# Kernel tuning notes

Measured on AMD Instinct MI355X. Metric: run time of the kernel, lower is better.

The kernel has to match this reference:

```python
import jax, jax.numpy as jnp
import numpy as np

TOP_K = 2
NUM_EXPERTS = 64
SEQ, BS, HS = 2048, 4, 4096
TOKENS = SEQ * BS  # tokens_per_batch
TOL = 1e-4
EPS = 1e-8


def sinkhorn(temp_cost):
    # temp_cost: (T, E) float32 logits. Mirrors SinkhornRouter.sinkhorn exactly.
    cost = jnp.exp(temp_cost)
    n0, n1 = cost.shape
    # initial d0 (overwritten inside loop in torch too, kept for fidelity of carry dtype/shape)
    d0 = (TOKENS / NUM_EXPERTS) * jnp.sum(jnp.exp(2.0 * temp_cost), axis=1)
    d1 = jnp.ones((n1,), dtype=cost.dtype)
    err0 = jnp.asarray(1e9, dtype=cost.dtype)

    def cond(carry):
        _, _, err = carry
        return err > TOL

    def body(carry):
        d0, d1, _ = carry  # d1 here plays the role of d1_old
        d0_new = (1.0 / n0) / (jnp.sum(d1 * cost, axis=1) + EPS)          # (T,)
        d1_new = (1.0 / n1) / (jnp.sum(d0_new[:, None] * cost, axis=0) + EPS)  # (E,)
        err = jnp.mean(jnp.abs(d1 - d1_new))
        return (d0_new, d1_new, err)

    d0, d1, _ = jax.lax.while_loop(cond, body, (d0, d1, err0))
    return d1 * cost * d0[:, None]


def setup_inputs() -> dict:
    key = jax.random.key(0)
    kx, kw = jax.random.split(key)
    x = jax.random.normal(kx, (SEQ, BS, HS), dtype=jnp.float32)
    W = jax.random.normal(kw, (NUM_EXPERTS, HS), dtype=jnp.float32) * 0.02
    return {"x": x, "W": W}


def reference(x, W):
    # router logits: (T, E)
    logits = jnp.reshape(x, (-1, x.shape[-1])) @ W.T
    # Sinkhorn normalization is done in fp32 under no_grad in torch -> stop_gradient
    norm_logits = sinkhorn(jax.lax.stop_gradient(logits).astype(jnp.float32))
    _, indices = jax.lax.top_k(norm_logits, TOP_K)  # (T, top_k) int32
    # top_k > 1 -> softmax activation (fp32, cast back)
    probs = jax.nn.softmax(logits.astype(jnp.float32), axis=-1).astype(logits.dtype)
    scores = jnp.take_along_axis(probs, indices, axis=1)  # (T, top_k)
    return scores, indices
```

## Files before the change

kernel.cpp:

```cpp
#include <hip/hip_runtime.h>
#include <hip/hip_cooperative_groups.h>
#include <math.h>

namespace cg = cooperative_groups;

namespace {
constexpr int kTokens = 8192;
constexpr int kHS = 4096;
constexpr float kTol = 1e-4f;
constexpr float kEps = 1e-8f;
constexpr int kMaxIters = 1000;
constexpr int kSinkBlocks = 64;
constexpr size_t kTagFloats = 128;
constexpr size_t kGdataFloats = 2 * 64 * 64;
constexpr size_t kPartOff = kTagFloats + kGdataFloats;
constexpr size_t kSliceFloats = (size_t)kTokens * 64;
constexpr size_t kWtpFloats = (size_t)(kHS / 4) * 64 * 4;
}

__device__ __forceinline__ float wave_sum(float v) {
#pragma unroll
  for (int o = 32; o; o >>= 1) v += __shfl_xor(v, o, 64);
  return v;
}

__global__ void __launch_bounds__(128, 2)
k_logits(const float* __restrict__ X, const float* __restrict__ W,
         float* __restrict__ part, int KS) {
  __shared__ float xs[32][132];
  __shared__ float wsh[32][68];
  const int tid = threadIdx.x;
  const int tx = tid & 7;
  const int ty = tid >> 3;
  const int tb = blockIdx.x & 63;
  const int s = blockIdx.x >> 6;
  const int t0 = tb * 128;
  const int k0 = s * KS;
  const int cx = tid & 7;
  const int rx = tid >> 3;

  const float* xsrc = X + (size_t)(t0 + rx) * kHS + k0 + 4 * cx;
  const float* wsrc = W + (size_t)rx * kHS + k0 + 4 * cx;

  float acc[8][8];
#pragma unroll
  for (int i = 0; i < 8; ++i)
#pragma unroll
    for (int j = 0; j < 8; ++j) acc[i][j] = 0.0f;

  const int nkt = KS / 32;
  float4 xa[8], wa[4];
#pragma unroll
  for (int p = 0; p < 8; ++p)
    xa[p] = *(const float4*)(xsrc + (size_t)p * 16 * kHS);
#pragma unroll
  for (int p = 0; p < 4; ++p)
    wa[p] = *(const float4*)(wsrc + (size_t)p * 16 * kHS);

  for (int kt = 0; kt < nkt; ++kt) {
    __syncthreads();
#pragma unroll
    for (int p = 0; p < 8; ++p) {
      xs[4 * cx + 0][rx + 16 * p] = xa[p].x;
      xs[4 * cx + 1][rx + 16 * p] = xa[p].y;
      xs[4 * cx + 2][rx + 16 * p] = xa[p].z;
      xs[4 * cx + 3][rx + 16 * p] = xa[p].w;
    }
#pragma unroll
    for (int p = 0; p < 4; ++p) {
      wsh[4 * cx + 0][rx + 16 * p] = wa[p].x;
      wsh[4 * cx + 1][rx + 16 * p] = wa[p].y;
      wsh[4 * cx + 2][rx + 16 * p] = wa[p].z;
      wsh[4 * cx + 3][rx + 16 * p] = wa[p].w;
    }
    __syncthreads();
    if (kt + 1 < nkt) {
      const int ko = (kt + 1) * 32;
#pragma unroll
      for (int p = 0; p < 8; ++p)
        xa[p] = *(const float4*)(xsrc + (size_t)p * 16 * kHS + ko);
#pragma unroll
      for (int p = 0; p < 4; ++p)
        wa[p] = *(const float4*)(wsrc + (size_t)p * 16 * kHS + ko);
    }
#pragma unroll 8
    for (int k = 0; k < 32; ++k) {
      const float4 x0 = *(const float4*)&xs[k][8 * ty];
      const float4 x1 = *(const float4*)&xs[k][8 * ty + 4];
      const float4 w0 = *(const float4*)&wsh[k][8 * tx];
      const float4 w1 = *(const float4*)&wsh[k][8 * tx + 4];
      const float xr[8] = {x0.x, x0.y, x0.z, x0.w, x1.x, x1.y, x1.z, x1.w};
      const float wr[8] = {w0.x, w0.y, w0.z, w0.w, w1.x, w1.y, w1.z, w1.w};
#pragma unroll
      for (int i = 0; i < 8; ++i)
#pragma unroll
        for (int j = 0; j < 8; ++j) acc[i][j] = fmaf(xr[i], wr[j], acc[i][j]);
    }
  }

  float* pb = part + ((size_t)s * kTokens + t0 + 8 * ty) * 64 + 8 * tx;
#pragma unroll
  for (int i = 0; i < 8; ++i) {
    *(float4*)(pb + (size_t)i * 64) =
        make_float4(acc[i][0], acc[i][1], acc[i][2], acc[i][3]);
    *(float4*)(pb + (size_t)i * 64 + 4) =
        make_float4(acc[i][4], acc[i][5], acc[i][6], acc[i][7]);
  }
}

__global__ void __launch_bounds__(1024, 1)
k_sinkhorn(const float* __restrict__ part, int S, float* __restrict__ out,
           unsigned* __restrict__ tags, float* __restrict__ gdata) {
  const int tid = threadIdx.x;
  const int lane = tid & 63;
  const int wid = __builtin_amdgcn_readfirstlane(tid >> 6);
  const int blk = blockIdx.x;
  __shared__ float lds[1024];

  const int t0 = blk * 128 + wid * 8;
  float lg[8], cst[8];
#pragma unroll
  for (int t = 0; t < 8; ++t) {
    float a = 0.0f;
    for (int s = 0; s < S; ++s)
      a += part[((size_t)s * kTokens + t0 + t) * 64 + lane];
    lg[t] = a;
    cst[t] = expf(a);
  }

  float d1 = 1.0f;
  float d0v[8];
  int buf = 0;
  for (int it = 0; it < kMaxIters; ++it) {
    float p = 0.0f;
#pragma unroll
    for (int t = 0; t < 8; ++t) {
      const float s = wave_sum(d1 * cst[t]);
      const float d0t = (1.0f / 8192.0f) / (s + kEps);
      d0v[t] = d0t;
      p = fmaf(d0t, cst[t], p);
    }
    __syncthreads();
    lds[wid * 64 + lane] = p;
    __syncthreads();
    const unsigned want = (unsigned)(it + 1);
    if (wid == 0) {
      float bp = 0.0f;
#pragma unroll
      for (int w = 0; w < 16; ++w) bp += lds[w * 64 + lane];
      __hip_atomic_store(&gdata[((size_t)buf * 64 + blk) * 64 + lane], bp,
                         __ATOMIC_RELAXED, __HIP_MEMORY_SCOPE_AGENT);
      __threadfence();
      if (lane == 0)
        __hip_atomic_store(&tags[buf * 64 + blk], want, __ATOMIC_RELEASE,
                           __HIP_MEMORY_SCOPE_AGENT);
      while (__hip_atomic_load(&tags[buf * 64 + lane], __ATOMIC_ACQUIRE,
                               __HIP_MEMORY_SCOPE_AGENT) != want) {
        __builtin_amdgcn_s_sleep(1);
      }
    }
    __syncthreads();
    float s2 = 0.0f;
#pragma unroll
    for (int i = 0; i < 4; ++i)
      s2 += __hip_atomic_load(
          &gdata[((size_t)buf * 64 + wid * 4 + i) * 64 + lane],
          __ATOMIC_RELAXED, __HIP_MEMORY_SCOPE_AGENT);
    lds[wid * 64 + lane] = s2;
    __syncthreads();
    float colsum = 0.0f;
#pragma unroll
    for (int w = 0; w < 16; ++w) colsum += lds[w * 64 + lane];
    const float d1n = (1.0f / 64.0f) / (colsum + kEps);
    const float err = wave_sum(fabsf(d1 - d1n)) * (1.0f / 64.0f);
    d1 = d1n;
    buf ^= 1;
    if (err <= kTol) break;
  }

#pragma unroll
  for (int t = 0; t < 8; ++t) {
    const float lgv = lg[t];
    float m = lgv;
#pragma unroll
    for (int o = 32; o; o >>= 1) m = fmaxf(m, __shfl_xor(m, o, 64));
    const float ex = expf(lgv - m);
    const float den = wave_sum(ex);
    const float prob = ex / den;

    const float v = (d1 * cst[t]) * d0v[t];
    float v1 = v;
    int i1 = lane;
#pragma unroll
    for (int o = 32; o; o >>= 1) {
      const float ov = __shfl_xor(v1, o, 64);
      const int oi = __shfl_xor(i1, o, 64);
      if (ov > v1 || (ov == v1 && oi < i1)) { v1 = ov; i1 = oi; }
    }
    float v2 = (lane == i1) ? -INFINITY : v;
    int i2 = lane;
#pragma unroll
    for (int o = 32; o; o >>= 1) {
      const float ov = __shfl_xor(v2, o, 64);
      const int oi = __shfl_xor(i2, o, 64);
      if (ov > v2 || (ov == v2 && oi < i2)) { v2 = ov; i2 = oi; }
    }
    const float p1 = __shfl(prob, i1, 64);
    const float p2 = __shfl(prob, i2, 64);
    if (lane == 0) {
      const int row = t0 + t;
      out[row * 2 + 0] = p1;
      out[row * 2 + 1] = p2;
      out[2 * kTokens + row * 2 + 0] = (float)i1;
      out[2 * kTokens + row * 2 + 1] = (float)i2;
    }
  }
}

__global__ void __launch_bounds__(256, 1)
sinkhorn_router(const float* __restrict__ X, const float* __restrict__ W,
                float* __restrict__ out, float* __restrict__ ws) {
  cg::grid_group grid = cg::this_grid();
  const int tid = threadIdx.x;
  const int lane = tid & 63;
  const int wid = __builtin_amdgcn_readfirstlane(tid >> 6);
  const int blk = blockIdx.x;

  float4* wtp = reinterpret_cast<float4*>(ws);
  float* gpart = ws + kWtpFloats;
  __shared__ float lds[256];

  {
    const int j = blk * 256 + tid;
    const int e = j & 63;
    const int k4 = j >> 6;
    wtp[j] = *reinterpret_cast<const float4*>(W + (size_t)e * kHS + 4 * (size_t)k4);
  }
  grid.sync();

  const int t0 = blk * 32 + wid * 8;
  const float* xb = X + (size_t)t0 * kHS;
  float lg[8];
#pragma unroll
  for (int t = 0; t < 8; ++t) lg[t] = 0.0f;

#pragma unroll 2
  for (int k4 = 0; k4 < kHS / 4; ++k4) {
    const float4 w = wtp[k4 * 64 + lane];
#pragma unroll
    for (int t = 0; t < 8; ++t) {
      const float* xr = xb + (size_t)t * kHS + 4 * (size_t)k4;
      float a = lg[t];
      a = fmaf(xr[0], w.x, a);
      a = fmaf(xr[1], w.y, a);
      a = fmaf(xr[2], w.z, a);
      a = fmaf(xr[3], w.w, a);
      lg[t] = a;
    }
  }

  float cst[8];
#pragma unroll
  for (int t = 0; t < 8; ++t) cst[t] = expf(lg[t]);

  float d1 = 1.0f;
  float d0v[8];
  int buf = 0;
  for (int it = 0; it < kMaxIters; ++it) {
    float p = 0.0f;
#pragma unroll
    for (int t = 0; t < 8; ++t) {
      const float s = wave_sum(d1 * cst[t]);
      const float d0t = (1.0f / 8192.0f) / (s + kEps);
      d0v[t] = d0t;
      p = fmaf(d0t, cst[t], p);
    }
    __syncthreads();
    lds[wid * 64 + lane] = p;
    __syncthreads();
    if (wid == 0) {
      const float bp =
          lds[lane] + lds[64 + lane] + lds[128 + lane] + lds[192 + lane];
      gpart[buf * (256 * 64) + blk * 64 + lane] = bp;
    }
    grid.sync();
    const float* gp = gpart + buf * (256 * 64);
    float s = 0.0f;
#pragma unroll 8
    for (int b = 0; b < 64; ++b) s += gp[(wid * 64 + b) * 64 + lane];
    lds[wid * 64 + lane] = s;
    __syncthreads();
    const float colsum =
        lds[lane] + lds[64 + lane] + lds[128 + lane] + lds[192 + lane];
    const float d1n = (1.0f / 64.0f) / (colsum + kEps);
    const float err = wave_sum(fabsf(d1 - d1n)) * (1.0f / 64.0f);
    d1 = d1n;
    buf ^= 1;
    if (err <= kTol) break;
  }

#pragma unroll
  for (int t = 0; t < 8; ++t) {
    const float lgv = lg[t];
    float m = lgv;
#pragma unroll
    for (int o = 32; o; o >>= 1) m = fmaxf(m, __shfl_xor(m, o, 64));
    const float ex = expf(lgv - m);
    const float den = wave_sum(ex);
    const float prob = ex / den;

    const float v = (d1 * cst[t]) * d0v[t];
    float v1 = v;
    int i1 = lane;
#pragma unroll
    for (int o = 32; o; o >>= 1) {
      const float ov = __shfl_xor(v1, o, 64);
      const int oi = __shfl_xor(i1, o, 64);
      if (ov > v1 || (ov == v1 && oi < i1)) { v1 = ov; i1 = oi; }
    }
    float v2 = (lane == i1) ? -INFINITY : v;
    int i2 = lane;
#pragma unroll
    for (int o = 32; o; o >>= 1) {
      const float ov = __shfl_xor(v2, o, 64);
      const int oi = __shfl_xor(i2, o, 64);
      if (ov > v2 || (ov == v2 && oi < i2)) { v2 = ov; i2 = oi; }
    }
    const float p1 = __shfl(prob, i1, 64);
    const float p2 = __shfl(prob, i2, 64);
    if (lane == 0) {
      const int row = t0 + t;
      out[row * 2 + 0] = p1;
      out[row * 2 + 1] = p2;
      out[2 * kTokens + row * 2 + 0] = (float)i1;
      out[2 * kTokens + row * 2 + 1] = (float)i2;
    }
  }
}

extern "C" void kernel_launch(void* const* d_in, const int* in_sizes, int n_in,
                              void* d_out, int out_size, void* d_ws,
                              size_t ws_size, hipStream_t stream) {
  const float* X = (const float*)d_in[0];
  const float* W = (const float*)d_in[1];
  float* out = (float*)d_out;
  float* ws = (float*)d_ws;

  int S = 0;
  for (int cand : {16, 8, 4, 2, 1}) {
    const size_t need = (kPartOff + (size_t)cand * kSliceFloats) * 4;
    if (need <= ws_size) { S = cand; break; }
  }

  if (S == 0) {
    void* args[] = {(void*)&X, (void*)&W, (void*)&out, (void*)&ws};
    hipLaunchCooperativeKernel((const void*)sinkhorn_router, dim3(256),
                               dim3(256), args, 0, stream);
    return;
  }

  unsigned* tags = reinterpret_cast<unsigned*>(ws);
  float* gdata = ws + kTagFloats;
  float* part = ws + kPartOff;

  const int KS = kHS / S;
  hipLaunchKernelGGL(k_logits, dim3(64 * S), dim3(128), 0, stream, X, W, part,
                     KS);
  hipLaunchKernelGGL(k_sinkhorn, dim3(kSinkBlocks), dim3(1024), 0, stream,
                     part, S, out, tags, gdata);
}
```

Baseline: 280.8 us.

## Compute router logits with split-bf16 MFMA and in-block split-K reduction

Replaces the FP32 SIMT GEMM that wrote per-slice partial logits with an MFMA kernel. Each FP32 input is split into bf16 hi and lo parts, and three bf16 MFMAs per tile emulate FP32 precision. Each block covers 32 tokens with 8 waves splitting K, and the wave partials are reduced in LDS so the full logits are written once. This removes the multi-slice partial buffer and the summation loop in the sinkhorn kernel. The cost is reduced precision (the lo*lo term is dropped), which could flip top-k choices near ties, and operands are read straight from global memory without LDS staging.

```diff
diff --git a/kernel.cpp b/kernel.cpp
--- a/kernel.cpp
+++ b/kernel.cpp
@@ -13,8 +13,8 @@
 constexpr int kSinkBlocks = 64;
 constexpr size_t kTagFloats = 128;
 constexpr size_t kGdataFloats = 2 * 64 * 64;
-constexpr size_t kPartOff = kTagFloats + kGdataFloats;
-constexpr size_t kSliceFloats = (size_t)kTokens * 64;
+constexpr size_t kLogitsOff = kTagFloats + kGdataFloats;
+constexpr size_t kLogitsFloats = (size_t)kTokens * 64;
 constexpr size_t kWtpFloats = (size_t)(kHS / 4) * 64 * 4;
 }
 
@@ -24,92 +24,93 @@
   return v;
 }
 
-__global__ void __launch_bounds__(128, 2)
+typedef __attribute__((ext_vector_type(8))) short bf16x8;
+typedef __attribute__((ext_vector_type(4))) float f32x4;
+
+__device__ __forceinline__ unsigned short f2bf(float x) {
+  unsigned u = __builtin_bit_cast(unsigned, x);
+  u += 0x7fffu + ((u >> 16) & 1u);
+  return (unsigned short)(u >> 16);
+}
+
+__device__ __forceinline__ void split8(const float* p, bf16x8& hi, bf16x8& lo) {
+  const float4 a = *(const float4*)p;
+  const float4 b = *(const float4*)(p + 4);
+  const float v[8] = {a.x, a.y, a.z, a.w, b.x, b.y, b.z, b.w};
+#pragma unroll
+  for (int j = 0; j < 8; ++j) {
+    const unsigned short h = f2bf(v[j]);
+    const float hf = __builtin_bit_cast(float, (unsigned)h << 16);
+    hi[j] = (short)h;
+    lo[j] = (short)f2bf(v[j] - hf);
+  }
+}
+
+__global__ void __launch_bounds__(512, 2)
 k_logits(const float* __restrict__ X, const float* __restrict__ W,
-         float* __restrict__ part, int KS) {
-  __shared__ float xs[32][132];
-  __shared__ float wsh[32][68];
+         float* __restrict__ logits) {
   const int tid = threadIdx.x;
-  const int tx = tid & 7;
-  const int ty = tid >> 3;
-  const int tb = blockIdx.x & 63;
-  const int s = blockIdx.x >> 6;
-  const int t0 = tb * 128;
-  const int k0 = s * KS;
-  const int cx = tid & 7;
-  const int rx = tid >> 3;
-
-  const float* xsrc = X + (size_t)(t0 + rx) * kHS + k0 + 4 * cx;
-  const float* wsrc = W + (size_t)rx * kHS + k0 + 4 * cx;
-
-  float acc[8][8];
-#pragma unroll
-  for (int i = 0; i < 8; ++i)
-#pragma unroll
-    for (int j = 0; j < 8; ++j) acc[i][j] = 0.0f;
-
-  const int nkt = KS / 32;
-  float4 xa[8], wa[4];
-#pragma unroll
-  for (int p = 0; p < 8; ++p)
-    xa[p] = *(const float4*)(xsrc + (size_t)p * 16 * kHS);
-#pragma unroll
-  for (int p = 0; p < 4; ++p)
-    wa[p] = *(const float4*)(wsrc + (size_t)p * 16 * kHS);
-
-  for (int kt = 0; kt < nkt; ++kt) {
-    __syncthreads();
-#pragma unroll
-    for (int p = 0; p < 8; ++p) {
-      xs[4 * cx + 0][rx + 16 * p] = xa[p].x;
-      xs[4 * cx + 1][rx + 16 * p] = xa[p].y;
-      xs[4 * cx + 2][rx + 16 * p] = xa[p].z;
-      xs[4 * cx + 3][rx + 16 * p] = xa[p].w;
-    }
-#pragma unroll
-    for (int p = 0; p < 4; ++p) {
-      wsh[4 * cx + 0][rx + 16 * p] = wa[p].x;
-      wsh[4 * cx + 1][rx + 16 * p] = wa[p].y;
-      wsh[4 * cx + 2][rx + 16 * p] = wa[p].z;
-      wsh[4 * cx + 3][rx + 16 * p] = wa[p].w;
-    }
-    __syncthreads();
-    if (kt + 1 < nkt) {
-      const int ko = (kt + 1) * 32;
-#pragma unroll
-      for (int p = 0; p < 8; ++p)
-        xa[p] = *(const float4*)(xsrc + (size_t)p * 16 * kHS + ko);
-#pragma unroll
-      for (int p = 0; p < 4; ++p)
-        wa[p] = *(const float4*)(wsrc + (size_t)p * 16 * kHS + ko);
-    }
-#pragma unroll 8
-    for (int k = 0; k < 32; ++k) {
-      const float4 x0 = *(const float4*)&xs[k][8 * ty];
-      const float4 x1 = *(const float4*)&xs[k][8 * ty + 4];
-      const float4 w0 = *(const float4*)&wsh[k][8 * tx];
-      const float4 w1 = *(const float4*)&wsh[k][8 * tx + 4];
-      const float xr[8] = {x0.x, x0.y, x0.z, x0.w, x1.x, x1.y, x1.z, x1.w};
-      const float wr[8] = {w0.x, w0.y, w0.z, w0.w, w1.x, w1.y, w1.z, w1.w};
-#pragma unroll
-      for (int i = 0; i < 8; ++i)
-#pragma unroll
-        for (int j = 0; j < 8; ++j) acc[i][j] = fmaf(xr[i], wr[j], acc[i][j]);
-    }
-  }
-
-  float* pb = part + ((size_t)s * kTokens + t0 + 8 * ty) * 64 + 8 * tx;
-#pragma unroll
-  for (int i = 0; i < 8; ++i) {
-    *(float4*)(pb + (size_t)i * 64) =
-        make_float4(acc[i][0], acc[i][1], acc[i][2], acc[i][3]);
-    *(float4*)(pb + (size_t)i * 64 + 4) =
-        make_float4(acc[i][4], acc[i][5], acc[i][6], acc[i][7]);
-  }
+  const int lane = tid & 63;
+  const int wid = tid >> 6;
+  const int t0 = blockIdx.x * 32;
+  const int r = lane & 15;
+  const int g = lane >> 4;
+
+  const float* xp = X + (size_t)(t0 + r) * kHS + wid * 512 + g * 8;
+  const float* wp = W + (size_t)r * kHS + wid * 512 + g * 8;
+
+  f32x4 acc[2][4];
+#pragma unroll
+  for (int m = 0; m < 2; ++m)
+#pragma unroll
+    for (int n = 0; n < 4; ++n) acc[m][n] = (f32x4){0.f, 0.f, 0.f, 0.f};
+
+#pragma unroll 2
+  for (int ks = 0; ks < 16; ++ks) {
+    const int ko = ks * 32;
+    bf16x8 ah[2], al[2], bh[4], bl[4];
+#pragma unroll
+    for (int m = 0; m < 2; ++m)
+      split8(xp + (size_t)(16 * m) * kHS + ko, ah[m], al[m]);
+#pragma unroll
+    for (int n = 0; n < 4; ++n)
+      split8(wp + (size_t)(16 * n) * kHS + ko, bh[n], bl[n]);
+#pragma unroll
+    for (int m = 0; m < 2; ++m)
+#pragma unroll
+      for (int n = 0; n < 4; ++n) {
+        acc[m][n] = __builtin_amdgcn_mfma_f32_16x16x32_bf16(ah[m], bh[n],
+                                                            acc[m][n], 0, 0, 0);
+        acc[m][n] = __builtin_amdgcn_mfma_f32_16x16x32_bf16(al[m], bh[n],
+                                                            acc[m][n], 0, 0, 0);
+        acc[m][n] = __builtin_amdgcn_mfma_f32_16x16x32_bf16(ah[m], bl[n],
+                                                            acc[m][n], 0, 0, 0);
+      }
+  }
+
+  __shared__ __align__(16) float red[8][32][68];
+#pragma unroll
+  for (int m = 0; m < 2; ++m)
+#pragma unroll
+    for (int n = 0; n < 4; ++n)
+#pragma unroll
+      for (int q = 0; q < 4; ++q)
+        red[wid][m * 16 + g * 4 + q][n * 16 + r] = acc[m][n][q];
+  __syncthreads();
+
+  const int t = tid >> 4;
+  const int e4 = (tid & 15) * 4;
+  float4 s = *(const float4*)&red[0][t][e4];
+#pragma unroll
+  for (int w = 1; w < 8; ++w) {
+    const float4 p = *(const float4*)&red[w][t][e4];
+    s.x += p.x; s.y += p.y; s.z += p.z; s.w += p.w;
+  }
+  *(float4*)(logits + (size_t)(t0 + t) * 64 + e4) = s;
 }
 
 __global__ void __launch_bounds__(1024, 1)
-k_sinkhorn(const float* __restrict__ part, int S, float* __restrict__ out,
+k_sinkhorn(const float* __restrict__ logits, float* __restrict__ out,
            unsigned* __restrict__ tags, float* __restrict__ gdata) {
   const int tid = threadIdx.x;
   const int lane = tid & 63;
@@ -121,9 +122,7 @@
   float lg[8], cst[8];
 #pragma unroll
   for (int t = 0; t < 8; ++t) {
-    float a = 0.0f;
-    for (int s = 0; s < S; ++s)
-      a += part[((size_t)s * kTokens + t0 + t) * 64 + lane];
+    const float a = logits[(size_t)(t0 + t) * 64 + lane];
     lg[t] = a;
     cst[t] = expf(a);
   }
@@ -346,13 +345,8 @@
   float* out = (float*)d_out;
   float* ws = (float*)d_ws;
 
-  int S = 0;
-  for (int cand : {16, 8, 4, 2, 1}) {
-    const size_t need = (kPartOff + (size_t)cand * kSliceFloats) * 4;
-    if (need <= ws_size) { S = cand; break; }
-  }
-
-  if (S == 0) {
+  const size_t need = (kLogitsOff + kLogitsFloats) * sizeof(float);
+  if (ws_size < need) {
     void* args[] = {(void*)&X, (void*)&W, (void*)&out, (void*)&ws};
     hipLaunchCooperativeKernel((const void*)sinkhorn_router, dim3(256),
                                dim3(256), args, 0, stream);
@@ -361,11 +355,10 @@
 
   unsigned* tags = reinterpret_cast<unsigned*>(ws);
   float* gdata = ws + kTagFloats;
-  float* part = ws + kPartOff;
-
-  const int KS = kHS / S;
-  hipLaunchKernelGGL(k_logits, dim3(64 * S), dim3(128), 0, stream, X, W, part,
-                     KS);
+  float* logits = ws + kLogitsOff;
+
+  hipLaunchKernelGGL(k_logits, dim3(kTokens / 32), dim3(512), 0, stream, X, W,
+                     logits);
   hipLaunchKernelGGL(k_sinkhorn, dim3(kSinkBlocks), dim3(1024), 0, stream,
-                     part, S, out, tags, gdata);
-}
+                     logits, out, tags, gdata);
+}
```

Result: faster. 269.0 us (-4.2%).
